# Performance work log

Hardware: AMD Instinct MI355X
Metric: run time of the kernel (lower is better)

The kernel has to match this reference:

```python
import jax, jax.numpy as jnp
import numpy as np

ALPHA = 1.0


def _bce_with_logits(x, y):
    # torch BCEWithLogitsLoss (mean): y*softplus(-x) + (1-y)*softplus(x)
    return jnp.mean(y * jax.nn.softplus(-x) + (1.0 - y) * jax.nn.softplus(x))


def _cross_entropy(logits, labels):
    # torch CrossEntropyLoss (mean) with int class labels
    logp = jax.nn.log_softmax(logits, axis=-1)
    return -jnp.mean(jnp.take_along_axis(logp, labels[:, None], axis=-1))


def setup_inputs() -> dict:
    key = jax.random.key(0)
    ks = jax.random.split(key, 6)
    B, T, C = 2097152, 4, 16
    return {
        "y_pred_binary": jax.random.normal(ks[0], (B,), dtype=jnp.float32),
        "y_pred_type": jax.random.normal(ks[1], (B, T), dtype=jnp.float32),
        "y_pred_source": jax.random.normal(ks[2], (B, C), dtype=jnp.float32),
        "y_true_binary": jnp.round(jax.random.uniform(ks[3], (B,), dtype=jnp.float32)),
        "y_true_type": jnp.round(jax.random.uniform(ks[4], (B, T), dtype=jnp.float32)),
        "y_true_source": jax.random.randint(ks[5], (B,), 0, C, dtype=jnp.int32),
    }


def reference(y_pred_binary, y_pred_type, y_pred_source,
              y_true_binary, y_true_type, y_true_source):
    loss = _bce_with_logits(y_pred_binary, y_true_binary)
    loss = loss + _bce_with_logits(y_pred_type, y_true_type)
    loss = loss + _cross_entropy(y_pred_source, y_true_source)

    # Non-differentiable consistency counts (torch computes these under
    # no_grad / via round+argmax, which carry no gradient).
    pb = jax.lax.stop_gradient(y_pred_binary)
    pt = jax.lax.stop_gradient(y_pred_type)
    ps = jax.lax.stop_gradient(y_pred_source)

    binary_c = jax.nn.sigmoid(pb) >= 0.5                     # [B] bool (round(sigmoid))
    type_c = jnp.any(jax.nn.sigmoid(pt) >= 0.5, axis=1)      # [B] bool
    source_c = jnp.argmax(ps, axis=1) > 0                    # [B] bool

    # XOR: exactly one of the pair active -> inconsistent
    cons_ab = jnp.mean((binary_c ^ type_c).astype(jnp.float32))
    cons_ac = jnp.mean((binary_c ^ source_c).astype(jnp.float32))

    loss = loss + ALPHA * cons_ab + ALPHA * cons_ac
    return loss
```

## Files before the change

### kernel.cpp

```cpp
#include <hip/hip_runtime.h>
#include <math.h>

__device__ __forceinline__ float softplus_f(float x) {
    return fmaxf(x, 0.0f) + log1pf(expf(-fabsf(x)));
}

__global__ __launch_bounds__(256) void multitask_loss_kernel(
    const float*  __restrict__ pb,
    const float4* __restrict__ pt,
    const float4* __restrict__ ps,
    const float*  __restrict__ tb,
    const float4* __restrict__ tt,
    const int*    __restrict__ ts,
    double*       __restrict__ acc,
    int B)
{
    int i = blockIdx.x * blockDim.x + threadIdx.x;
    float contrib = 0.0f;
    if (i < B) {
        float x = pb[i];
        float y = tb[i];
        contrib = softplus_f(x) - y * x;
        bool bin_c = (x >= 0.0f);

        float4 xt = pt[i];
        float4 yt = tt[i];
        float tsum = (softplus_f(xt.x) - yt.x * xt.x)
                   + (softplus_f(xt.y) - yt.y * xt.y)
                   + (softplus_f(xt.z) - yt.z * xt.z)
                   + (softplus_f(xt.w) - yt.w * xt.w);
        contrib += 0.25f * tsum;
        bool type_c = (xt.x >= 0.0f) || (xt.y >= 0.0f) ||
                      (xt.z >= 0.0f) || (xt.w >= 0.0f);

        size_t base = (size_t)i * 4;
        float4 r0 = ps[base + 0];
        float4 r1 = ps[base + 1];
        float4 r2 = ps[base + 2];
        float4 r3 = ps[base + 3];
        float v[16] = { r0.x, r0.y, r0.z, r0.w,
                        r1.x, r1.y, r1.z, r1.w,
                        r2.x, r2.y, r2.z, r2.w,
                        r3.x, r3.y, r3.z, r3.w };
        float m = v[0];
        #pragma unroll
        for (int j = 1; j < 16; ++j) m = fmaxf(m, v[j]);
        float s = 0.0f;
        #pragma unroll
        for (int j = 0; j < 16; ++j) s += expf(v[j] - m);
        int lab = ts[i];
        float vlab = v[0];
        #pragma unroll
        for (int j = 1; j < 16; ++j) vlab = (lab == j) ? v[j] : vlab;
        contrib += m + logf(s) - vlab;

        float max_rest = v[1];
        #pragma unroll
        for (int j = 2; j < 16; ++j) max_rest = fmaxf(max_rest, v[j]);
        bool src_c = (max_rest > v[0]);

        contrib += (bin_c != type_c) ? 1.0f : 0.0f;
        contrib += (bin_c != src_c)  ? 1.0f : 0.0f;
    }

    #pragma unroll
    for (int off = 32; off > 0; off >>= 1)
        contrib += __shfl_down(contrib, off, 64);

    __shared__ float wsum[4];
    int lane = threadIdx.x & 63;
    int wave = threadIdx.x >> 6;
    if (lane == 0) wsum[wave] = contrib;
    __syncthreads();
    if (threadIdx.x == 0) {
        float bsum = wsum[0] + wsum[1] + wsum[2] + wsum[3];
        atomicAdd(acc, (double)bsum);
    }
}

__global__ void finalize_kernel(const double* __restrict__ acc,
                                float* __restrict__ out, double invB) {
    out[0] = (float)(acc[0] * invB);
}

extern "C" void kernel_launch(void* const* d_in, const int* in_sizes, int n_in,
                              void* d_out, int out_size, void* d_ws, size_t ws_size,
                              hipStream_t stream) {
    const float*  pb = (const float*)d_in[0];
    const float4* pt = (const float4*)d_in[1];
    const float4* ps = (const float4*)d_in[2];
    const float*  tb = (const float*)d_in[3];
    const float4* tt = (const float4*)d_in[4];
    const int*    ts = (const int*)d_in[5];
    int B = in_sizes[0];

    double* acc = (double*)d_ws;
    hipMemsetAsync(d_ws, 0, sizeof(double), stream);

    int blocks = (B + 255) / 256;
    multitask_loss_kernel<<<blocks, 256, 0, stream>>>(pb, pt, ps, tb, tt, ts, acc, B);
    finalize_kernel<<<1, 1, 0, stream>>>(acc, (float*)d_out, 1.0 / (double)B);
}
```

Measured before the change: 295.0 us.

## Process four rows per thread, use fast math, replace atomics with two-pass reduction

Each thread now handles four rows and reads the binary and label arrays as float4/int4 vectors. Per-block double atomicAdd and the memset are replaced by a partials array and a single-block reduction kernel. Softplus, exp and log use the fast __expf/__logf intrinsics. The kernel assumes B is divisible by 4 and loses some accuracy from the intrinsics. Per-thread loads of ps are strided by 256 bytes across threads, which could hurt coalescing.

After: 271.6 us. -8.0%, faster.

```diff
diff --git a/kernel.cpp b/kernel.cpp
--- a/kernel.cpp
+++ b/kernel.cpp
@@ -1,66 +1,81 @@
 #include <hip/hip_runtime.h>
 #include <math.h>
 
-__device__ __forceinline__ float softplus_f(float x) {
-    return fmaxf(x, 0.0f) + log1pf(expf(-fabsf(x)));
+__device__ __forceinline__ float fast_softplus(float x) {
+    return fmaxf(x, 0.0f) + __logf(1.0f + __expf(-fabsf(x)));
+}
+
+__device__ __forceinline__ float row_contrib(float xb, float yb,
+                                             float4 xt, float4 yt,
+                                             const float v[16], int lab)
+{
+    float c = fast_softplus(xb) - yb * xb;
+    bool bin_c = (xb >= 0.0f);
+
+    float tsum = (fast_softplus(xt.x) - yt.x * xt.x)
+               + (fast_softplus(xt.y) - yt.y * xt.y)
+               + (fast_softplus(xt.z) - yt.z * xt.z)
+               + (fast_softplus(xt.w) - yt.w * xt.w);
+    c += 0.25f * tsum;
+    bool type_c = (xt.x >= 0.0f) || (xt.y >= 0.0f) ||
+                  (xt.z >= 0.0f) || (xt.w >= 0.0f);
+
+    float m = v[0];
+    #pragma unroll
+    for (int j = 1; j < 16; ++j) m = fmaxf(m, v[j]);
+    float s = 0.0f;
+    #pragma unroll
+    for (int j = 0; j < 16; ++j) s += __expf(v[j] - m);
+    float vlab = v[0];
+    #pragma unroll
+    for (int j = 1; j < 16; ++j) vlab = (lab == j) ? v[j] : vlab;
+    c += m + __logf(s) - vlab;
+
+    float mr = v[1];
+    #pragma unroll
+    for (int j = 2; j < 16; ++j) mr = fmaxf(mr, v[j]);
+    bool src_c = (mr > v[0]);
+
+    c += (bin_c != type_c) ? 1.0f : 0.0f;
+    c += (bin_c != src_c)  ? 1.0f : 0.0f;
+    return c;
 }
 
 __global__ __launch_bounds__(256) void multitask_loss_kernel(
-    const float*  __restrict__ pb,
-    const float4* __restrict__ pt,
-    const float4* __restrict__ ps,
-    const float*  __restrict__ tb,
-    const float4* __restrict__ tt,
-    const int*    __restrict__ ts,
-    double*       __restrict__ acc,
-    int B)
+    const float4* __restrict__ pb4,
+    const float4* __restrict__ pt4,
+    const float4* __restrict__ ps4,
+    const float4* __restrict__ tb4,
+    const float4* __restrict__ tt4,
+    const int4*   __restrict__ ts4,
+    float*        __restrict__ partials,
+    int n4)
 {
-    int i = blockIdx.x * blockDim.x + threadIdx.x;
+    int t = blockIdx.x * blockDim.x + threadIdx.x;
     float contrib = 0.0f;
-    if (i < B) {
-        float x = pb[i];
-        float y = tb[i];
-        contrib = softplus_f(x) - y * x;
-        bool bin_c = (x >= 0.0f);
+    if (t < n4) {
+        float4 xb = pb4[t];
+        float4 yb = tb4[t];
+        int4   lb = ts4[t];
+        float xbv[4] = { xb.x, xb.y, xb.z, xb.w };
+        float ybv[4] = { yb.x, yb.y, yb.z, yb.w };
+        int   lbv[4] = { lb.x, lb.y, lb.z, lb.w };
 
-        float4 xt = pt[i];
-        float4 yt = tt[i];
-        float tsum = (softplus_f(xt.x) - yt.x * xt.x)
-                   + (softplus_f(xt.y) - yt.y * xt.y)
-                   + (softplus_f(xt.z) - yt.z * xt.z)
-                   + (softplus_f(xt.w) - yt.w * xt.w);
-        contrib += 0.25f * tsum;
-        bool type_c = (xt.x >= 0.0f) || (xt.y >= 0.0f) ||
-                      (xt.z >= 0.0f) || (xt.w >= 0.0f);
-
-        size_t base = (size_t)i * 4;
-        float4 r0 = ps[base + 0];
-        float4 r1 = ps[base + 1];
-        float4 r2 = ps[base + 2];
-        float4 r3 = ps[base + 3];
-        float v[16] = { r0.x, r0.y, r0.z, r0.w,
-                        r1.x, r1.y, r1.z, r1.w,
-                        r2.x, r2.y, r2.z, r2.w,
-                        r3.x, r3.y, r3.z, r3.w };
-        float m = v[0];
         #pragma unroll
-        for (int j = 1; j < 16; ++j) m = fmaxf(m, v[j]);
-        float s = 0.0f;
-        #pragma unroll
-        for (int j = 0; j < 16; ++j) s += expf(v[j] - m);
-        int lab = ts[i];
-        float vlab = v[0];
-        #pragma unroll
-        for (int j = 1; j < 16; ++j) vlab = (lab == j) ? v[j] : vlab;
-        contrib += m + logf(s) - vlab;
-
-        float max_rest = v[1];
-        #pragma unroll
-        for (int j = 2; j < 16; ++j) max_rest = fmaxf(max_rest, v[j]);
-        bool src_c = (max_rest > v[0]);
-
-        contrib += (bin_c != type_c) ? 1.0f : 0.0f;
-        contrib += (bin_c != src_c)  ? 1.0f : 0.0f;
+        for (int k = 0; k < 4; ++k) {
+            float4 xt = pt4[(size_t)t * 4 + k];
+            float4 yt = tt4[(size_t)t * 4 + k];
+            size_t base = (size_t)t * 16 + (size_t)k * 4;
+            float4 r0 = ps4[base + 0];
+            float4 r1 = ps4[base + 1];
+            float4 r2 = ps4[base + 2];
+            float4 r3 = ps4[base + 3];
+            float v[16] = { r0.x, r0.y, r0.z, r0.w,
+                            r1.x, r1.y, r1.z, r1.w,
+                            r2.x, r2.y, r2.z, r2.w,
+                            r3.x, r3.y, r3.z, r3.w };
+            contrib += row_contrib(xbv[k], ybv[k], xt, yt, v, lbv[k]);
+        }
     }
 
     #pragma unroll
@@ -72,32 +87,48 @@
     int wave = threadIdx.x >> 6;
     if (lane == 0) wsum[wave] = contrib;
     __syncthreads();
-    if (threadIdx.x == 0) {
-        float bsum = wsum[0] + wsum[1] + wsum[2] + wsum[3];
-        atomicAdd(acc, (double)bsum);
-    }
+    if (threadIdx.x == 0)
+        partials[blockIdx.x] = wsum[0] + wsum[1] + wsum[2] + wsum[3];
 }
 
-__global__ void finalize_kernel(const double* __restrict__ acc,
-                                float* __restrict__ out, double invB) {
-    out[0] = (float)(acc[0] * invB);
+__global__ __launch_bounds__(256) void reduce_kernel(
+    const float* __restrict__ partials, int n,
+    float* __restrict__ out, double invB)
+{
+    double s = 0.0;
+    for (int i = threadIdx.x; i < n; i += 256)
+        s += (double)partials[i];
+
+    #pragma unroll
+    for (int off = 32; off > 0; off >>= 1)
+        s += __shfl_down(s, off, 64);
+
+    __shared__ double wsum[4];
+    int lane = threadIdx.x & 63;
+    int wave = threadIdx.x >> 6;
+    if (lane == 0) wsum[wave] = s;
+    __syncthreads();
+    if (threadIdx.x == 0)
+        out[0] = (float)((wsum[0] + wsum[1] + wsum[2] + wsum[3]) * invB);
 }
 
 extern "C" void kernel_launch(void* const* d_in, const int* in_sizes, int n_in,
                               void* d_out, int out_size, void* d_ws, size_t ws_size,
                               hipStream_t stream) {
-    const float*  pb = (const float*)d_in[0];
-    const float4* pt = (const float4*)d_in[1];
-    const float4* ps = (const float4*)d_in[2];
-    const float*  tb = (const float*)d_in[3];
-    const float4* tt = (const float4*)d_in[4];
-    const int*    ts = (const int*)d_in[5];
+    const float4* pb4 = (const float4*)d_in[0];
+    const float4* pt4 = (const float4*)d_in[1];
+    const float4* ps4 = (const float4*)d_in[2];
+    const float4* tb4 = (const float4*)d_in[3];
+    const float4* tt4 = (const float4*)d_in[4];
+    const int4*   ts4 = (const int4*)d_in[5];
     int B = in_sizes[0];
+    int n4 = B / 4;
 
-    double* acc = (double*)d_ws;
-    hipMemsetAsync(d_ws, 0, sizeof(double), stream);
+    float* partials = (float*)d_ws;
 
-    int blocks = (B + 255) / 256;
-    multitask_loss_kernel<<<blocks, 256, 0, stream>>>(pb, pt, ps, tb, tt, ts, acc, B);
-    finalize_kernel<<<1, 1, 0, stream>>>(acc, (float*)d_out, 1.0 / (double)B);
+    int blocks = (n4 + 255) / 256;
+    multitask_loss_kernel<<<blocks, 256, 0, stream>>>(pb4, pt4, ps4, tb4, tt4, ts4,
+                                                      partials, n4);
+    reduce_kernel<<<1, 256, 0, stream>>>(partials, blocks, (float*)d_out,
+                                         1.0 / (double)B);
 }
```
